# Kernel optimization log

Hardware: AMD Instinct MI355X
Metric: run time of the kernel (lower is better)

The kernel has to match this reference:

```python
import jax, jax.numpy as jnp
import numpy as np

IN_C, HID, OUT_C = 768, 568, 1024
EPS = 1e-5

def _ln(x, g, b):
    mu = jnp.mean(x, axis=-1, keepdims=True)
    var = jnp.var(x, axis=-1, keepdims=True)
    return (x - mu) / jnp.sqrt(var + EPS) * g + b

def setup_inputs() -> dict:
    key = jax.random.key(0)
    ks = jax.random.split(key, 20)
    def lin(k, fan_in, fan_out):
        bound = 1.0 / np.sqrt(fan_in)
        kw, kb = jax.random.split(k)
        w = jax.random.uniform(kw, (fan_in, fan_out), jnp.float32, -bound, bound)
        b = jax.random.uniform(kb, (fan_out,), jnp.float32, -bound, bound)
        return w, b
    x = jax.random.normal(ks[0], (4, 2048, IN_C), jnp.float32)
    w_mlp, b_mlp = lin(ks[1], IN_C, HID)
    wq, bq = lin(ks[2], HID, OUT_C)
    wk, bk = lin(ks[3], HID, OUT_C)
    wv, bv = lin(ks[4], HID, OUT_C)
    wm, bm = lin(ks[5], HID, OUT_C)
    wf1, bf1 = lin(ks[6], OUT_C, OUT_C)
    wf2, bf2 = lin(ks[7], OUT_C, OUT_C)
    g1 = jnp.ones((OUT_C,), jnp.float32); be1 = jnp.zeros((OUT_C,), jnp.float32)
    g2 = jnp.ones((OUT_C,), jnp.float32); be2 = jnp.zeros((OUT_C,), jnp.float32)
    return dict(x=x, w_mlp=w_mlp, b_mlp=b_mlp, wq=wq, bq=bq, wk=wk, bk=bk,
                wv=wv, bv=bv, wm=wm, bm=bm, g1=g1, be1=be1,
                wf1=wf1, bf1=bf1, wf2=wf2, bf2=bf2, g2=g2, be2=be2)

def reference(x, w_mlp, b_mlp, wq, bq, wk, bk, wv, bv, wm, bm,
              g1, be1, wf1, bf1, wf2, bf2, g2, be2):
    # Joint.mlp: Linear + ReLU  -> h: [B, S, HID]
    h = jax.nn.relu(jnp.einsum('bsi,ih->bsh', x, w_mlp) + b_mlp)
    # Block: single-head attention (dropout=eval -> identity)
    q = jnp.einsum('bsh,hd->bsd', h, wq) + bq
    k = jnp.einsum('bsh,hd->bsd', h, wk) + bk
    v = jnp.einsum('bsh,hd->bsd', h, wv) + bv
    scale = 1.0 / jnp.sqrt(jnp.float32(OUT_C))
    attn = jax.nn.softmax(jnp.einsum('bqd,bkd->bqk', q, k) * scale, axis=-1)
    attn_out = jnp.einsum('bqk,bkd->bqd', attn, v)
    x_mod = jnp.einsum('bsh,hd->bsd', h, wm) + bm
    x1 = _ln(x_mod + attn_out, g1, be1)
    ffn = jnp.einsum('bsd,de->bse', jax.nn.relu(jnp.einsum('bsd,de->bse', x1, wf1) + bf1), wf2) + bf2
    x2 = _ln(x1 + ffn, g2, be2)
    # trailing ReLU in Joint.attn Sequential
    return jax.nn.relu(x2)
```

## Files before the change

### kernel.cpp

```cpp
#include <hip/hip_runtime.h>

#define DI __device__ __forceinline__

typedef unsigned short u16;
typedef __attribute__((__ext_vector_type__(8))) __bf16 bf16x8;
typedef __attribute__((__ext_vector_type__(4))) float f32x4;
typedef __attribute__((__ext_vector_type__(4))) unsigned short u16x4;
typedef __attribute__((__ext_vector_type__(8))) unsigned short u16x8;

DI float bf2f(u16 u) { union { unsigned int i; float f; } x; x.i = ((unsigned int)u) << 16; return x.f; }
DI u16 f2bf(float f) {
  union { float f; unsigned int i; } x; x.f = f;
  unsigned int r = x.i + 0x7fffu + ((x.i >> 16) & 1u);
  return (u16)(r >> 16);
}

DI void gload_lds16(const void* g, void* lds) {
  __builtin_amdgcn_global_load_lds((const __attribute__((address_space(1))) unsigned int*)g,
                                   (__attribute__((address_space(3))) unsigned int*)lds, 16, 0, 0);
}

template<bool RELU, bool OUT_BF16, bool HAS_BIAS>
__global__ __launch_bounds__(512, 2)
void gemm256v2(const u16* __restrict__ A, long long sAb, int lda,
               const u16* __restrict__ Bt, long long sBb, int ldb,
               const float* __restrict__ bias,
               void* __restrict__ C, long long sCb, int ldc,
               int K, float scale)
{
  extern __shared__ __align__(16) u16 lds[];

  const int tid = threadIdx.x;
  const int w = tid >> 6, l = tid & 63;
  const int wm = w >> 2, wn = w & 3;

  const int gx = gridDim.x;
  const int nwg = gx * gridDim.y;
  const int f = blockIdx.x + gx * blockIdx.y;
  const int fs = (f & 7) * (nwg >> 3) + (f >> 3);
  const int bx = fs % gx, by = fs / gx;

  const long long bm = (long long)by * 256;
  const long long bn = (long long)bx * 256;
  const u16* Ab = A + (long long)blockIdx.z * sAb;
  const u16* Btb = Bt + (long long)blockIdx.z * sBb;

  const int trow = tid >> 3;
  const int tg = (tid & 7) ^ (trow & 7);
  const u16* sA = Ab + (bm + trow) * (long long)lda + tg * 8;
  const u16* sB = Btb + (bn + trow) * (long long)ldb + tg * 8;
  const long long la64 = (long long)64 * lda, lb64 = (long long)64 * ldb;

  const int swz0 = (((l >> 4) ^ (l & 7))) * 8;
  const int aB = (wm * 128 + (l & 15)) * 64;
  const int bB = 16384 + (wn * 64 + (l & 15)) * 64;

  f32x4 acc[8][4] = {};
  const int NKT = K >> 6;

  {
    u16* sp = lds;
    gload_lds16(sA, sp + w * 512);
    gload_lds16(sA + 2 * la64, sp + 8192 + w * 512);
    gload_lds16(sB, sp + 16384 + w * 512);
    gload_lds16(sB + lb64, sp + 20480 + w * 512);
    gload_lds16(sB + 2 * lb64, sp + 24576 + w * 512);
    gload_lds16(sB + 3 * lb64, sp + 28672 + w * 512);
    gload_lds16(sA + la64, sp + 4096 + w * 512);
    gload_lds16(sA + 3 * la64, sp + 12288 + w * 512);
  }

  for (int kt = 0; kt < NKT; ++kt) {
    const u16* bp = lds + (kt & 1) * 32768;
    u16* sp = lds + ((kt & 1) ^ 1) * 32768;
    const bool st = (kt + 1) < NKT;
    const long long ko = (long long)(kt + 1) * 64;

    asm volatile("s_waitcnt vmcnt(2)" ::: "memory");
    __builtin_amdgcn_s_barrier();

    if (st) {
      gload_lds16(sA + ko, sp + w * 512);
      gload_lds16(sA + 2 * la64 + ko, sp + 8192 + w * 512);
      gload_lds16(sB + ko, sp + 16384 + w * 512);
      gload_lds16(sB + lb64 + ko, sp + 20480 + w * 512);
      gload_lds16(sB + 2 * lb64 + ko, sp + 24576 + w * 512);
      gload_lds16(sB + 3 * lb64 + ko, sp + 28672 + w * 512);
    }

    bf16x8 bF[4][2], aF[4][2];
    #pragma unroll
    for (int nf = 0; nf < 4; ++nf) {
      bF[nf][0] = *(const bf16x8*)(bp + bB + nf * 1024 + swz0);
      bF[nf][1] = *(const bf16x8*)(bp + bB + nf * 1024 + (swz0 ^ 32));
    }
    #pragma unroll
    for (int mf = 0; mf < 4; ++mf) {
      aF[mf][0] = *(const bf16x8*)(bp + aB + mf * 1024 + swz0);
      aF[mf][1] = *(const bf16x8*)(bp + aB + mf * 1024 + (swz0 ^ 32));
    }
    if (st) {
      gload_lds16(sA + la64 + ko, sp + 4096 + w * 512);
      gload_lds16(sA + 3 * la64 + ko, sp + 12288 + w * 512);
    }
    __builtin_amdgcn_s_setprio(1);
    #pragma unroll
    for (int mf = 0; mf < 4; ++mf)
      #pragma unroll
      for (int nf = 0; nf < 4; ++nf) {
        acc[mf][nf] = __builtin_amdgcn_mfma_f32_16x16x32_bf16(aF[mf][0], bF[nf][0], acc[mf][nf], 0, 0, 0);
        acc[mf][nf] = __builtin_amdgcn_mfma_f32_16x16x32_bf16(aF[mf][1], bF[nf][1], acc[mf][nf], 0, 0, 0);
      }
    __builtin_amdgcn_s_setprio(0);

    if (st) asm volatile("s_waitcnt vmcnt(8)" ::: "memory");
    else    asm volatile("s_waitcnt vmcnt(0)" ::: "memory");
    __builtin_amdgcn_s_barrier();

    #pragma unroll
    for (int mf = 0; mf < 4; ++mf) {
      aF[mf][0] = *(const bf16x8*)(bp + aB + (mf + 4) * 1024 + swz0);
      aF[mf][1] = *(const bf16x8*)(bp + aB + (mf + 4) * 1024 + (swz0 ^ 32));
    }
    __builtin_amdgcn_s_setprio(1);
    #pragma unroll
    for (int mf = 0; mf < 4; ++mf)
      #pragma unroll
      for (int nf = 0; nf < 4; ++nf) {
        acc[mf + 4][nf] = __builtin_amdgcn_mfma_f32_16x16x32_bf16(aF[mf][0], bF[nf][0], acc[mf + 4][nf], 0, 0, 0);
        acc[mf + 4][nf] = __builtin_amdgcn_mfma_f32_16x16x32_bf16(aF[mf][1], bF[nf][1], acc[mf + 4][nf], 0, 0, 0);
      }
    __builtin_amdgcn_s_setprio(0);
  }

  __syncthreads();
  float bias4[4];
  if (HAS_BIAS) {
    #pragma unroll
    for (int nf = 0; nf < 4; ++nf) bias4[nf] = bias[bn + wn * 64 + (l & 15) + nf * 16];
  }
  float* fl = (float*)lds + w * 1024;
  const long long cbase = (long long)blockIdx.z * sCb;
  const int colq = (l & 15) * 4;
  #pragma unroll
  for (int mf = 0; mf < 8; ++mf) {
    #pragma unroll
    for (int nf = 0; nf < 4; ++nf) {
      #pragma unroll
      for (int r = 0; r < 4; ++r) {
        float v = acc[mf][nf][r] * scale;
        if (HAS_BIAS) v += bias4[nf];
        if (RELU) v = fmaxf(v, 0.f);
        fl[((l >> 4) * 4 + r) * 64 + (l & 15) + nf * 16] = v;
      }
    }
    asm volatile("s_waitcnt lgkmcnt(0)" ::: "memory");
    #pragma unroll
    for (int p = 0; p < 4; ++p) {
      f32x4 v = *(const f32x4*)(fl + p * 256 + l * 4);
      const long long row = bm + wm * 128 + mf * 16 + p * 4 + (l >> 4);
      const long long cidx = cbase + row * ldc + bn + wn * 64 + colq;
      if (OUT_BF16) {
        u16x4 o; o.x = f2bf(v.x); o.y = f2bf(v.y); o.z = f2bf(v.z); o.w = f2bf(v.w);
        *(u16x4*)((u16*)C + cidx) = o;
      } else {
        *(f32x4*)((float*)C + cidx) = v;
      }
    }
    asm volatile("s_waitcnt lgkmcnt(0)" ::: "memory");
  }
}

template<bool RELU, bool OUT_BF16, bool HAS_BIAS>
__global__ __launch_bounds__(512, 4)
void gemm128(const u16* __restrict__ A, long long sAb, int lda,
             const u16* __restrict__ Bt, long long sBb, int ldb,
             const float* __restrict__ bias,
             void* __restrict__ C, long long sCb, int ldc,
             int K, float scale)
{
  __shared__ __align__(16) u16 lds[24576];

  const int tid = threadIdx.x;
  const int w = tid >> 6, l = tid & 63;
  const int wm = w >> 2, wn = w & 3;

  const int gx = gridDim.x;
  const int nwg = gx * gridDim.y;
  const int f = blockIdx.x + gx * blockIdx.y;
  const int fs = (f & 7) * (nwg >> 3) + (f >> 3);
  const int bx = fs % gx, by = fs / gx;

  const long long bm = (long long)by * 128;
  const long long bn = (long long)bx * 256;
  const u16* Ab = A + (long long)blockIdx.z * sAb;
  const u16* Btb = Bt + (long long)blockIdx.z * sBb;

  const int ia = w * 64 + l;
  const int ra = ia >> 2;
  const int ga = (ia & 3) ^ ((ra >> 1) & 3);
  const u16* pA  = Ab  + (bm + ra) * (long long)lda + ga * 8;
  const u16* pB0 = Btb + (bn + ra) * (long long)ldb + ga * 8;
  const u16* pB1 = Btb + (bn + 128 + ra) * (long long)ldb + ga * 8;
  u16* dA  = lds + w * 512;
  u16* dB0 = lds + 4096 + w * 512;
  u16* dB1 = lds + 8192 + w * 512;

  const int swz = ((l >> 4) ^ (((l & 15) >> 1) & 3)) << 3;
  const int aOff = (wm * 64 + (l & 15)) * 32 + swz;
  const int bOff = 4096 + (wn * 64 + (l & 15)) * 32 + swz;

  f32x4 acc[4][4] = {};
  const int NKT = K >> 5;

  gload_lds16(pA, dA);        gload_lds16(pB0, dB0);        gload_lds16(pB1, dB1);
  gload_lds16(pA + 32, dA + 12288); gload_lds16(pB0 + 32, dB0 + 12288); gload_lds16(pB1 + 32, dB1 + 12288);

  for (int kt = 0; kt < NKT; ++kt) {
    if (kt + 1 < NKT) asm volatile("s_waitcnt vmcnt(3)" ::: "memory");
    else              asm volatile("s_waitcnt vmcnt(0)" ::: "memory");
    __builtin_amdgcn_s_barrier();
    __builtin_amdgcn_sched_barrier(0);

    const u16* bufc = lds + (kt & 1) * 12288;
    bf16x8 aF[4], bF[4];
    #pragma unroll
    for (int mf = 0; mf < 4; ++mf) aF[mf] = *(const bf16x8*)(bufc + aOff + mf * 512);
    #pragma unroll
    for (int nf = 0; nf < 4; ++nf) bF[nf] = *(const bf16x8*)(bufc + bOff + nf * 512);
    asm volatile("s_waitcnt lgkmcnt(0)" ::: "memory");
    __builtin_amdgcn_s_barrier();
    __builtin_amdgcn_sched_barrier(0);

    if (kt + 2 < NKT) {
      u16* d = lds + (kt & 1) * 12288 + w * 512;
      const long long ko = (long long)(kt + 2) * 32;
      gload_lds16(pA + ko, d);
      gload_lds16(pB0 + ko, d + 4096);
      gload_lds16(pB1 + ko, d + 8192);
    }
    __builtin_amdgcn_s_setprio(1);
    #pragma unroll
    for (int mf = 0; mf < 4; ++mf)
      #pragma unroll
      for (int nf = 0; nf < 4; ++nf)
        acc[mf][nf] = __builtin_amdgcn_mfma_f32_16x16x32_bf16(aF[mf], bF[nf], acc[mf][nf], 0, 0, 0);
    __builtin_amdgcn_s_setprio(0);
  }

  float bias4[4];
  if (HAS_BIAS) {
    #pragma unroll
    for (int nf = 0; nf < 4; ++nf) bias4[nf] = bias[bn + wn * 64 + (l & 15) + nf * 16];
  }
  float* fl = (float*)lds + w * 1024;
  const long long cbase = (long long)blockIdx.z * sCb;
  const int colq = (l & 15) * 4;
  #pragma unroll
  for (int mf = 0; mf < 4; ++mf) {
    #pragma unroll
    for (int nf = 0; nf < 4; ++nf) {
      #pragma unroll
      for (int r = 0; r < 4; ++r) {
        float v = acc[mf][nf][r] * scale;
        if (HAS_BIAS) v += bias4[nf];
        if (RELU) v = fmaxf(v, 0.f);
        fl[((l >> 4) * 4 + r) * 64 + (l & 15) + nf * 16] = v;
      }
    }
    asm volatile("s_waitcnt lgkmcnt(0)" ::: "memory");
    #pragma unroll
    for (int p = 0; p < 4; ++p) {
      f32x4 v = *(const f32x4*)(fl + p * 256 + l * 4);
      const long long row = bm + wm * 64 + mf * 16 + p * 4 + (l >> 4);
      const long long cidx = cbase + row * ldc + bn + wn * 64 + colq;
      if (OUT_BF16) {
        u16x4 o; o.x = f2bf(v.x); o.y = f2bf(v.y); o.z = f2bf(v.z); o.w = f2bf(v.w);
        *(u16x4*)((u16*)C + cidx) = o;
      } else {
        *(f32x4*)((float*)C + cidx) = v;
      }
    }
    asm volatile("s_waitcnt lgkmcnt(0)" ::: "memory");
  }
}

__global__ void transpose_cast_pad(const float* __restrict__ in, int inR, int inC,
                                   u16* __restrict__ out, int outR, int outC)
{
  __shared__ float tile[32][33];
  const int c0 = blockIdx.x * 32;
  const int r0 = blockIdx.y * 32;
  const int tx = threadIdx.x, ty = threadIdx.y;
  for (int i = ty; i < 32; i += 8) {
    int r = r0 + i, c = c0 + tx;
    tile[i][tx] = (r < inR && c < inC) ? in[(long long)r * inC + c] : 0.f;
  }
  __syncthreads();
  for (int i = ty; i < 32; i += 8) {
    int orow = c0 + i, ocol = r0 + tx;
    if (orow < outR && ocol < outC)
      out[(long long)orow * outC + ocol] = f2bf(tile[tx][i]);
  }
}

__global__ void transpose_bf16_k(const u16* __restrict__ in, long long sIb, int ldi,
                                 u16* __restrict__ out, long long sOb, int ldo)
{
  __shared__ u16 tile[32][33];
  const u16* inp = in + (long long)blockIdx.z * sIb;
  u16* outp = out + (long long)blockIdx.z * sOb;
  const int r0 = blockIdx.y * 32, c0 = blockIdx.x * 32;
  const int tx = threadIdx.x, ty = threadIdx.y;
  for (int i = ty; i < 32; i += 8)
    tile[i][tx] = inp[(long long)(r0 + i) * ldi + c0 + tx];
  __syncthreads();
  for (int i = ty; i < 32; i += 8)
    outp[(long long)(c0 + i) * ldo + r0 + tx] = tile[tx][i];
}

__global__ void cast_f32_bf16_k(const float* __restrict__ in, u16* __restrict__ out, int n4)
{
  int i = blockIdx.x * blockDim.x + threadIdx.x;
  if (i >= n4) return;
  float4 v = ((const float4*)in)[i];
  u16x4 o; o.x = f2bf(v.x); o.y = f2bf(v.y); o.z = f2bf(v.z); o.w = f2bf(v.w);
  ((u16x4*)out)[i] = o;
}

__global__ void prep_bias_k(const float* __restrict__ bmlp, const float* __restrict__ bq,
                            const float* __restrict__ bk, const float* __restrict__ bv,
                            const float* __restrict__ bm,
                            float* __restrict__ outMlp, float* __restrict__ outQkvm)
{
  int i = blockIdx.x * 256 + threadIdx.x;
  if (i < 768) outMlp[i] = (i < 568) ? bmlp[i] : 0.f;
  if (i < 4096) {
    const float* s = (i < 1024) ? bq : (i < 2048) ? bk : (i < 3072) ? bv : bm;
    outQkvm[i] = s[i & 1023];
  }
}

__global__ __launch_bounds__(256)
void softmax_rows_k(u16* __restrict__ sc)
{
  __shared__ float red[8];
  const long long base = (long long)blockIdx.x * 2048;
  const int t = threadIdx.x, wave = t >> 6, lane = t & 63;
  u16x8 v8 = *((const u16x8*)(sc + base + t * 8));
  float v[8];
  #pragma unroll
  for (int j = 0; j < 8; ++j) v[j] = bf2f(v8[j]);
  float m = v[0];
  #pragma unroll
  for (int j = 1; j < 8; ++j) m = fmaxf(m, v[j]);
  #pragma unroll
  for (int off = 32; off > 0; off >>= 1) m = fmaxf(m, __shfl_xor(m, off, 64));
  if (lane == 0) red[wave] = m;
  __syncthreads();
  m = fmaxf(fmaxf(red[0], red[1]), fmaxf(red[2], red[3]));
  float s = 0.f;
  #pragma unroll
  for (int j = 0; j < 8; ++j) { v[j] = __expf(v[j] - m); s += v[j]; }
  #pragma unroll
  for (int off = 32; off > 0; off >>= 1) s += __shfl_xor(s, off, 64);
  if (lane == 0) red[4 + wave] = s;
  __syncthreads();
  s = red[4] + red[5] + red[6] + red[7];
  float inv = 1.f / s;
  u16x8 o;
  #pragma unroll
  for (int j = 0; j < 8; ++j) o[j] = f2bf(v[j] * inv);
  *((u16x8*)(sc + base + t * 8)) = o;
}

__global__ __launch_bounds__(256)
void add_ln_k(const u16* __restrict__ a, int lda, const float* __restrict__ b,
              const float* __restrict__ gamma, const float* __restrict__ beta,
              u16* __restrict__ out)
{
  __shared__ float red[8];
  const long long row = blockIdx.x;
  const int t = threadIdx.x, wave = t >> 6, lane = t & 63;
  u16x4 av = *((const u16x4*)(a + row * lda + t * 4));
  float4 bv = ((const float4*)(b + row * 1024))[t];
  float z[4] = { bf2f(av.x) + bv.x, bf2f(av.y) + bv.y, bf2f(av.z) + bv.z, bf2f(av.w) + bv.w };
  float s = z[0] + z[1] + z[2] + z[3];
  float ss = z[0]*z[0] + z[1]*z[1] + z[2]*z[2] + z[3]*z[3];
  #pragma unroll
  for (int off = 32; off > 0; off >>= 1) { s += __shfl_xor(s, off, 64); ss += __shfl_xor(ss, off, 64); }
  if (lane == 0) { red[wave] = s; red[4 + wave] = ss; }
  __syncthreads();
  s = red[0] + red[1] + red[2] + red[3];
  ss = red[4] + red[5] + red[6] + red[7];
  float mu = s * (1.f / 1024.f);
  float var = ss * (1.f / 1024.f) - mu * mu;
  float rstd = rsqrtf(var + 1e-5f);
  float4 g = ((const float4*)gamma)[t];
  float4 be = ((const float4*)beta)[t];
  u16x4 o;
  o.x = f2bf((z[0] - mu) * rstd * g.x + be.x);
  o.y = f2bf((z[1] - mu) * rstd * g.y + be.y);
  o.z = f2bf((z[2] - mu) * rstd * g.z + be.z);
  o.w = f2bf((z[3] - mu) * rstd * g.w + be.w);
  *((u16x4*)(out + row * 1024 + t * 4)) = o;
}

__global__ __launch_bounds__(256)
void add_ln_relu_k(const u16* __restrict__ a, const float* __restrict__ b,
                   const float* __restrict__ gamma, const float* __restrict__ beta,
                   float* __restrict__ out)
{
  __shared__ float red[8];
  const long long row = blockIdx.x;
  const int t = threadIdx.x, wave = t >> 6, lane = t & 63;
  u16x4 av = *((const u16x4*)(a + row * 1024 + t * 4));
  float4 bv = ((const float4*)(b + row * 1024))[t];
  float z[4] = { bf2f(av.x) + bv.x, bf2f(av.y) + bv.y, bf2f(av.z) + bv.z, bf2f(av.w) + bv.w };
  float s = z[0] + z[1] + z[2] + z[3];
  float ss = z[0]*z[0] + z[1]*z[1] + z[2]*z[2] + z[3]*z[3];
  #pragma unroll
  for (int off = 32; off > 0; off >>= 1) { s += __shfl_xor(s, off, 64); ss += __shfl_xor(ss, off, 64); }
  if (lane == 0) { red[wave] = s; red[4 + wave] = ss; }
  __syncthreads();
  s = red[0] + red[1] + red[2] + red[3];
  ss = red[4] + red[5] + red[6] + red[7];
  float mu = s * (1.f / 1024.f);
  float var = ss * (1.f / 1024.f) - mu * mu;
  float rstd = rsqrtf(var + 1e-5f);
  float4 g = ((const float4*)gamma)[t];
  float4 be = ((const float4*)beta)[t];
  float4 o;
  o.x = fmaxf((z[0] - mu) * rstd * g.x + be.x, 0.f);
  o.y = fmaxf((z[1] - mu) * rstd * g.y + be.y, 0.f);
  o.z = fmaxf((z[2] - mu) * rstd * g.z + be.z, 0.f);
  o.w = fmaxf((z[3] - mu) * rstd * g.w + be.w, 0.f);
  ((float4*)(out + row * 1024))[t] = o;
}

extern "C" void kernel_launch(void* const* d_in, const int* in_sizes, int n_in,
                              void* d_out, int out_size, void* d_ws, size_t ws_size,
                              hipStream_t stream)
{
  const float* x    = (const float*)d_in[0];
  const float* wmlp = (const float*)d_in[1];
  const float* bmlp = (const float*)d_in[2];
  const float* wq   = (const float*)d_in[3];  const float* bq  = (const float*)d_in[4];
  const float* wk   = (const float*)d_in[5];  const float* bk  = (const float*)d_in[6];
  const float* wv   = (const float*)d_in[7];  const float* bv  = (const float*)d_in[8];
  const float* wm   = (const float*)d_in[9];  const float* bm  = (const float*)d_in[10];
  const float* g1   = (const float*)d_in[11]; const float* be1 = (const float*)d_in[12];
  const float* wf1  = (const float*)d_in[13]; const float* bf1 = (const float*)d_in[14];
  const float* wf2  = (const float*)d_in[15]; const float* bf2 = (const float*)d_in[16];
  const float* g2   = (const float*)d_in[17]; const float* be2 = (const float*)d_in[18];

  char* ws = (char*)d_ws;
  size_t off = 0;
  auto alloc = [&](size_t bytes) { char* p = ws + off; off += (bytes + 255) & ~(size_t)255; return p; };
  u16*  W_MLP_T  = (u16*)alloc((size_t)768 * 768 * 2);
  u16*  W_QKVM_T = (u16*)alloc((size_t)4096 * 640 * 2);
  u16*  W_F1_T   = (u16*)alloc((size_t)1024 * 1024 * 2);
  u16*  W_F2_T   = (u16*)alloc((size_t)1024 * 1024 * 2);
  float* B_MLP   = (float*)alloc(768 * 4);
  float* B_QKVM  = (float*)alloc(4096 * 4);
  u16*  XBF      = (u16*)alloc((size_t)8192 * 768 * 2);
  u16*  H        = (u16*)alloc((size_t)8192 * 768 * 2);
  u16*  QKVM     = (u16*)alloc((size_t)8192 * 4096 * 2);
  u16*  VT       = (u16*)alloc((size_t)4 * 1024 * 2048 * 2);
  u16*  SC       = (u16*)alloc((size_t)4 * 2048 * 2048 * 2);
  float* AO      = (float*)alloc((size_t)8192 * 1024 * 4);
  u16*  X1       = (u16*)alloc((size_t)8192 * 1024 * 2);
  u16*  T  = QKVM;
  float* F = (float*)((char*)QKVM + (size_t)8192 * 2048 * 2);

  hipFuncSetAttribute((const void*)gemm256v2<false, true, true >, hipFuncAttributeMaxDynamicSharedMemorySize, 131072);
  hipFuncSetAttribute((const void*)gemm256v2<false, true, false>, hipFuncAttributeMaxDynamicSharedMemorySize, 131072);

  dim3 tb(32, 8);

  cast_f32_bf16_k<<<(8192 * 768 / 4 + 255) / 256, 256, 0, stream>>>(x, XBF, 8192 * 768 / 4);
  transpose_cast_pad<<<dim3(24, 24), tb, 0, stream>>>(wmlp, 768, 568, W_MLP_T, 768, 768);
  transpose_cast_pad<<<dim3(32, 20), tb, 0, stream>>>(wq, 568, 1024, W_QKVM_T + (size_t)0 * 1024 * 640, 1024, 640);
  transpose_cast_pad<<<dim3(32, 20), tb, 0, stream>>>(wk, 568, 1024, W_QKVM_T + (size_t)1 * 1024 * 640, 1024, 640);
  transpose_cast_pad<<<dim3(32, 20), tb, 0, stream>>>(wv, 568, 1024, W_QKVM_T + (size_t)2 * 1024 * 640, 1024, 640);
  transpose_cast_pad<<<dim3(32, 20), tb, 0, stream>>>(wm, 568, 1024, W_QKVM_T + (size_t)3 * 1024 * 640, 1024, 640);
  transpose_cast_pad<<<dim3(32, 32), tb, 0, stream>>>(wf1, 1024, 1024, W_F1_T, 1024, 1024);
  transpose_cast_pad<<<dim3(32, 32), tb, 0, stream>>>(wf2, 1024, 1024, W_F2_T, 1024, 1024);
  prep_bias_k<<<16, 256, 0, stream>>>(bmlp, bq, bk, bv, bm, B_MLP, B_QKVM);

  gemm128<true, true, true><<<dim3(3, 64, 1), 512, 0, stream>>>(
      XBF, 0, 768, W_MLP_T, 0, 768, B_MLP, H, 0, 768, 768, 1.0f);
  gemm256v2<false, true, true><<<dim3(16, 32, 1), 512, 131072, stream>>>(
      H, 0, 768, W_QKVM_T, 0, 640, B_QKVM, QKVM, 0, 4096, 640, 1.0f);
  transpose_bf16_k<<<dim3(32, 64, 4), tb, 0, stream>>>(
      QKVM + 2048, (long long)2048 * 4096, 4096, VT, (long long)1024 * 2048, 2048);
  gemm256v2<false, true, false><<<dim3(8, 8, 4), 512, 131072, stream>>>(
      QKVM, (long long)2048 * 4096, 4096, QKVM + 1024, (long long)2048 * 4096, 4096,
      nullptr, SC, (long long)2048 * 2048, 2048, 1024, 0.03125f);
  softmax_rows_k<<<8192, 256, 0, stream>>>(SC);
  gemm128<false, false, false><<<dim3(4, 16, 4), 512, 0, stream>>>(
      SC, (long long)2048 * 2048, 2048, VT, (long long)1024 * 2048, 2048,
      nullptr, AO, (long long)2048 * 1024, 1024, 2048, 1.0f);
  add_ln_k<<<8192, 256, 0, stream>>>(QKVM + 3072, 4096, AO, g1, be1, X1);
  gemm128<true, true, true><<<dim3(4, 64, 1), 512, 0, stream>>>(
      X1, 0, 1024, W_F1_T, 0, 1024, bf1, T, 0, 1024, 1024, 1.0f);
  gemm128<false, false, true><<<dim3(4, 64, 1), 512, 0, stream>>>(
      T, 0, 1024, W_F2_T, 0, 1024, bf2, F, 0, 1024, 1024, 1.0f);
  add_ln_relu_k<<<8192, 256, 0, stream>>>(X1, F, g2, be2, (float*)d_out);
}
```

Measured before the change: 281.2 us.

## Restructure 256-tile GEMM into 8-phase pipeline, swizzle epilogue LDS, store bf16 intermediates

The 256x256 GEMM main loop is split into four sub-phases per K tile, each loading two A fragments and issuing staggered global-to-LDS prefetches, with B prefetched two tiles ahead. The goal is to interleave memory traffic with MFMA work more finely. Both GEMM epilogues now XOR-swizzle the LDS staging buffer to avoid bank conflicts. The attention output and FFN2 output are written as bf16 instead of fp32, halving their traffic into the layernorm kernels at the cost of some precision.

```diff
diff --git a/kernel.cpp b/kernel.cpp
--- a/kernel.cpp
+++ b/kernel.cpp
@@ -20,13 +20,15 @@
                                    (__attribute__((address_space(3))) unsigned int*)lds, 16, 0, 0);
 }
 
+#define MFMA16(a, b, c) __builtin_amdgcn_mfma_f32_16x16x32_bf16((a), (b), (c), 0, 0, 0)
+
 template<bool RELU, bool OUT_BF16, bool HAS_BIAS>
 __global__ __launch_bounds__(512, 2)
-void gemm256v2(const u16* __restrict__ A, long long sAb, int lda,
-               const u16* __restrict__ Bt, long long sBb, int ldb,
-               const float* __restrict__ bias,
-               void* __restrict__ C, long long sCb, int ldc,
-               int K, float scale)
+void gemm8p(const u16* __restrict__ A, long long sAb, int lda,
+            const u16* __restrict__ Bt, long long sBb, int ldb,
+            const float* __restrict__ bias,
+            void* __restrict__ C, long long sCb, int ldc,
+            int K, float scale)
 {
   extern __shared__ __align__(16) u16 lds[];
 
@@ -47,93 +49,132 @@
 
   const int trow = tid >> 3;
   const int tg = (tid & 7) ^ (trow & 7);
-  const u16* sA = Ab + (bm + trow) * (long long)lda + tg * 8;
-  const u16* sB = Btb + (bn + trow) * (long long)ldb + tg * 8;
-  const long long la64 = (long long)64 * lda, lb64 = (long long)64 * ldb;
-
-  const int swz0 = (((l >> 4) ^ (l & 7))) * 8;
-  const int aB = (wm * 128 + (l & 15)) * 64;
-  const int bB = 16384 + (wn * 64 + (l & 15)) * 64;
+  const u16* gA = Ab + (bm + trow) * (long long)lda + tg * 8;
+  const u16* gB = Btb + (bn + trow) * (long long)ldb + tg * 8;
+  const long long a64 = (long long)64 * lda, b64 = (long long)64 * ldb;
+  const int wlds = w * 512;
+
+  const int slot0 = ((l >> 4) ^ (l & 7)) * 8;
+  const int aRow = (wm * 128 + (l & 15)) * 64;
+  const int bRow = 16384 + (wn * 64 + (l & 15)) * 64;
 
   f32x4 acc[8][4] = {};
   const int NKT = K >> 6;
 
-  {
-    u16* sp = lds;
-    gload_lds16(sA, sp + w * 512);
-    gload_lds16(sA + 2 * la64, sp + 8192 + w * 512);
-    gload_lds16(sB, sp + 16384 + w * 512);
-    gload_lds16(sB + lb64, sp + 20480 + w * 512);
-    gload_lds16(sB + 2 * lb64, sp + 24576 + w * 512);
-    gload_lds16(sB + 3 * lb64, sp + 28672 + w * 512);
-    gload_lds16(sA + la64, sp + 4096 + w * 512);
-    gload_lds16(sA + 3 * la64, sp + 12288 + w * 512);
-  }
-
-  for (int kt = 0; kt < NKT; ++kt) {
-    const u16* bp = lds + (kt & 1) * 32768;
-    u16* sp = lds + ((kt & 1) ^ 1) * 32768;
-    const bool st = (kt + 1) < NKT;
-    const long long ko = (long long)(kt + 1) * 64;
-
-    asm volatile("s_waitcnt vmcnt(2)" ::: "memory");
-    __builtin_amdgcn_s_barrier();
-
-    if (st) {
-      gload_lds16(sA + ko, sp + w * 512);
-      gload_lds16(sA + 2 * la64 + ko, sp + 8192 + w * 512);
-      gload_lds16(sB + ko, sp + 16384 + w * 512);
-      gload_lds16(sB + lb64 + ko, sp + 20480 + w * 512);
-      gload_lds16(sB + 2 * lb64 + ko, sp + 24576 + w * 512);
-      gload_lds16(sB + 3 * lb64 + ko, sp + 28672 + w * 512);
+  gload_lds16(gB,             lds + 16384 + wlds);
+  gload_lds16(gB + b64,       lds + 16384 + 4096 + wlds);
+  gload_lds16(gB + 2 * b64,   lds + 16384 + 8192 + wlds);
+  gload_lds16(gB + 3 * b64,   lds + 16384 + 12288 + wlds);
+  gload_lds16(gA,             lds + wlds);
+  gload_lds16(gA + a64,       lds + 4096 + wlds);
+  gload_lds16(gA + 2 * a64,   lds + 8192 + wlds);
+  gload_lds16(gA + 3 * a64,   lds + 12288 + wlds);
+  if (NKT > 1) {
+    gload_lds16(gB + 64,           lds + 32768 + 16384 + wlds);
+    gload_lds16(gB + b64 + 64,     lds + 32768 + 16384 + 4096 + wlds);
+    gload_lds16(gB + 2 * b64 + 64, lds + 32768 + 16384 + 8192 + wlds);
+    gload_lds16(gB + 3 * b64 + 64, lds + 32768 + 16384 + 12288 + wlds);
+    asm volatile("s_waitcnt vmcnt(4)" ::: "memory");
+  } else {
+    asm volatile("s_waitcnt vmcnt(0)" ::: "memory");
+  }
+  __builtin_amdgcn_s_barrier();
+
+  for (int t = 0; t < NKT; ++t) {
+    const u16* bp = lds + (t & 1) * 32768;
+    u16* cur = lds + (t & 1) * 32768;
+    u16* oth = lds + ((t + 1) & 1) * 32768;
+    const long long koA = (long long)(t + 1) * 64;
+    const long long koB = (long long)(t + 2) * 64;
+    const bool stA = (t + 1) < NKT;
+    const bool stB = (t + 2) < NKT;
+
+    bf16x8 bF[4][2], aF[2][2];
+
+    #pragma unroll
+    for (int nf = 0; nf < 4; ++nf) {
+      bF[nf][0] = *(const bf16x8*)(bp + bRow + nf * 1024 + slot0);
+      bF[nf][1] = *(const bf16x8*)(bp + bRow + nf * 1024 + (slot0 ^ 32));
     }
-
-    bf16x8 bF[4][2], aF[4][2];
-    #pragma unroll
-    for (int nf = 0; nf < 4; ++nf) {
-      bF[nf][0] = *(const bf16x8*)(bp + bB + nf * 1024 + swz0);
-      bF[nf][1] = *(const bf16x8*)(bp + bB + nf * 1024 + (swz0 ^ 32));
-    }
-    #pragma unroll
-    for (int mf = 0; mf < 4; ++mf) {
-      aF[mf][0] = *(const bf16x8*)(bp + aB + mf * 1024 + swz0);
-      aF[mf][1] = *(const bf16x8*)(bp + aB + mf * 1024 + (swz0 ^ 32));
-    }
-    if (st) {
-      gload_lds16(sA + la64 + ko, sp + 4096 + w * 512);
-      gload_lds16(sA + 3 * la64 + ko, sp + 12288 + w * 512);
-    }
+    aF[0][0] = *(const bf16x8*)(bp + aRow + slot0);
+    aF[0][1] = *(const bf16x8*)(bp + aRow + (slot0 ^ 32));
+    aF[1][0] = *(const bf16x8*)(bp + aRow + 1024 + slot0);
+    aF[1][1] = *(const bf16x8*)(bp + aRow + 1024 + (slot0 ^ 32));
+    if (stA) { gload_lds16(gA + koA, oth + wlds); gload_lds16(gA + a64 + koA, oth + 4096 + wlds); }
+    __builtin_amdgcn_s_barrier();
+    asm volatile("s_waitcnt lgkmcnt(0)" ::: "memory");
+    __builtin_amdgcn_sched_barrier(0);
     __builtin_amdgcn_s_setprio(1);
     #pragma unroll
-    for (int mf = 0; mf < 4; ++mf)
+    for (int mf = 0; mf < 2; ++mf)
       #pragma unroll
       for (int nf = 0; nf < 4; ++nf) {
-        acc[mf][nf] = __builtin_amdgcn_mfma_f32_16x16x32_bf16(aF[mf][0], bF[nf][0], acc[mf][nf], 0, 0, 0);
-        acc[mf][nf] = __builtin_amdgcn_mfma_f32_16x16x32_bf16(aF[mf][1], bF[nf][1], acc[mf][nf], 0, 0, 0);
+        acc[mf][nf] = MFMA16(aF[mf][0], bF[nf][0], acc[mf][nf]);
+        acc[mf][nf] = MFMA16(aF[mf][1], bF[nf][1], acc[mf][nf]);
       }
     __builtin_amdgcn_s_setprio(0);
-
-    if (st) asm volatile("s_waitcnt vmcnt(8)" ::: "memory");
-    else    asm volatile("s_waitcnt vmcnt(0)" ::: "memory");
-    __builtin_amdgcn_s_barrier();
-
-    #pragma unroll
-    for (int mf = 0; mf < 4; ++mf) {
-      aF[mf][0] = *(const bf16x8*)(bp + aB + (mf + 4) * 1024 + swz0);
-      aF[mf][1] = *(const bf16x8*)(bp + aB + (mf + 4) * 1024 + (swz0 ^ 32));
-    }
+    __builtin_amdgcn_s_barrier();
+
+    aF[0][0] = *(const bf16x8*)(bp + aRow + 2048 + slot0);
+    aF[0][1] = *(const bf16x8*)(bp + aRow + 2048 + (slot0 ^ 32));
+    aF[1][0] = *(const bf16x8*)(bp + aRow + 3072 + slot0);
+    aF[1][1] = *(const bf16x8*)(bp + aRow + 3072 + (slot0 ^ 32));
+    if (stA) { gload_lds16(gA + 2 * a64 + koA, oth + 8192 + wlds); gload_lds16(gA + 3 * a64 + koA, oth + 12288 + wlds); }
+    __builtin_amdgcn_s_barrier();
+    asm volatile("s_waitcnt lgkmcnt(0)" ::: "memory");
+    __builtin_amdgcn_sched_barrier(0);
     __builtin_amdgcn_s_setprio(1);
     #pragma unroll
-    for (int mf = 0; mf < 4; ++mf)
+    for (int mf = 0; mf < 2; ++mf)
       #pragma unroll
       for (int nf = 0; nf < 4; ++nf) {
-        acc[mf + 4][nf] = __builtin_amdgcn_mfma_f32_16x16x32_bf16(aF[mf][0], bF[nf][0], acc[mf + 4][nf], 0, 0, 0);
-        acc[mf + 4][nf] = __builtin_amdgcn_mfma_f32_16x16x32_bf16(aF[mf][1], bF[nf][1], acc[mf + 4][nf], 0, 0, 0);
+        acc[mf + 2][nf] = MFMA16(aF[mf][0], bF[nf][0], acc[mf + 2][nf]);
+        acc[mf + 2][nf] = MFMA16(aF[mf][1], bF[nf][1], acc[mf + 2][nf]);
       }
     __builtin_amdgcn_s_setprio(0);
-  }
-
-  __syncthreads();
+    __builtin_amdgcn_s_barrier();
+
+    aF[0][0] = *(const bf16x8*)(bp + aRow + 4096 + slot0);
+    aF[0][1] = *(const bf16x8*)(bp + aRow + 4096 + (slot0 ^ 32));
+    aF[1][0] = *(const bf16x8*)(bp + aRow + 5120 + slot0);
+    aF[1][1] = *(const bf16x8*)(bp + aRow + 5120 + (slot0 ^ 32));
+    if (stB) { gload_lds16(gB + koB, cur + 16384 + wlds); gload_lds16(gB + b64 + koB, cur + 16384 + 4096 + wlds); }
+    __builtin_amdgcn_s_barrier();
+    asm volatile("s_waitcnt lgkmcnt(0)" ::: "memory");
+    __builtin_amdgcn_sched_barrier(0);
+    __builtin_amdgcn_s_setprio(1);
+    #pragma unroll
+    for (int mf = 0; mf < 2; ++mf)
+      #pragma unroll
+      for (int nf = 0; nf < 4; ++nf) {
+        acc[mf + 4][nf] = MFMA16(aF[mf][0], bF[nf][0], acc[mf + 4][nf]);
+        acc[mf + 4][nf] = MFMA16(aF[mf][1], bF[nf][1], acc[mf + 4][nf]);
+      }
+    __builtin_amdgcn_s_setprio(0);
+    __builtin_amdgcn_s_barrier();
+
+    aF[0][0] = *(const bf16x8*)(bp + aRow + 6144 + slot0);
+    aF[0][1] = *(const bf16x8*)(bp + aRow + 6144 + (slot0 ^ 32));
+    aF[1][0] = *(const bf16x8*)(bp + aRow + 7168 + slot0);
+    aF[1][1] = *(const bf16x8*)(bp + aRow + 7168 + (slot0 ^ 32));
+    if (stB) { gload_lds16(gB + 2 * b64 + koB, cur + 16384 + 8192 + wlds); gload_lds16(gB + 3 * b64 + koB, cur + 16384 + 12288 + wlds); }
+    __builtin_amdgcn_s_barrier();
+    asm volatile("s_waitcnt lgkmcnt(0)" ::: "memory");
+    __builtin_amdgcn_sched_barrier(0);
+    __builtin_amdgcn_s_setprio(1);
+    #pragma unroll
+    for (int mf = 0; mf < 2; ++mf)
+      #pragma unroll
+      for (int nf = 0; nf < 4; ++nf) {
+        acc[mf + 6][nf] = MFMA16(aF[mf][0], bF[nf][0], acc[mf + 6][nf]);
+        acc[mf + 6][nf] = MFMA16(aF[mf][1], bF[nf][1], acc[mf + 6][nf]);
+      }
+    __builtin_amdgcn_s_setprio(0);
+    if (stB)      asm volatile("s_waitcnt vmcnt(4)" ::: "memory");
+    else if (stA) asm volatile("s_waitcnt vmcnt(0)" ::: "memory");
+    __builtin_amdgcn_s_barrier();
+  }
+
   float bias4[4];
   if (HAS_BIAS) {
     #pragma unroll
@@ -141,7 +182,7 @@
   }
   float* fl = (float*)lds + w * 1024;
   const long long cbase = (long long)blockIdx.z * sCb;
-  const int colq = (l & 15) * 4;
+  const int q = l >> 4;
   #pragma unroll
   for (int mf = 0; mf < 8; ++mf) {
     #pragma unroll
@@ -151,15 +192,15 @@
         float v = acc[mf][nf][r] * scale;
         if (HAS_BIAS) v += bias4[nf];
         if (RELU) v = fmaxf(v, 0.f);
-        fl[((l >> 4) * 4 + r) * 64 + (l & 15) + nf * 16] = v;
+        fl[(q * 4 + r) * 64 + ((((l & 15) + nf * 16)) ^ (q << 4))] = v;
       }
     }
     asm volatile("s_waitcnt lgkmcnt(0)" ::: "memory");
     #pragma unroll
     for (int p = 0; p < 4; ++p) {
-      f32x4 v = *(const f32x4*)(fl + p * 256 + l * 4);
-      const long long row = bm + wm * 128 + mf * 16 + p * 4 + (l >> 4);
-      const long long cidx = cbase + row * ldc + bn + wn * 64 + colq;
+      f32x4 v = *(const f32x4*)(fl + (p * 4 + q) * 64 + (((l & 15) * 4) ^ (p << 4)));
+      const long long row = bm + wm * 128 + mf * 16 + p * 4 + q;
+      const long long cidx = cbase + row * ldc + bn + wn * 64 + (l & 15) * 4;
       if (OUT_BF16) {
         u16x4 o; o.x = f2bf(v.x); o.y = f2bf(v.y); o.z = f2bf(v.z); o.w = f2bf(v.w);
         *(u16x4*)((u16*)C + cidx) = o;
@@ -244,7 +285,7 @@
     for (int mf = 0; mf < 4; ++mf)
       #pragma unroll
       for (int nf = 0; nf < 4; ++nf)
-        acc[mf][nf] = __builtin_amdgcn_mfma_f32_16x16x32_bf16(aF[mf], bF[nf], acc[mf][nf], 0, 0, 0);
+        acc[mf][nf] = MFMA16(aF[mf], bF[nf], acc[mf][nf]);
     __builtin_amdgcn_s_setprio(0);
   }
 
@@ -255,7 +296,7 @@
   }
   float* fl = (float*)lds + w * 1024;
   const long long cbase = (long long)blockIdx.z * sCb;
-  const int colq = (l & 15) * 4;
+  const int q = l >> 4;
   #pragma unroll
   for (int mf = 0; mf < 4; ++mf) {
     #pragma unroll
@@ -265,15 +306,15 @@
         float v = acc[mf][nf][r] * scale;
         if (HAS_BIAS) v += bias4[nf];
         if (RELU) v = fmaxf(v, 0.f);
-        fl[((l >> 4) * 4 + r) * 64 + (l & 15) + nf * 16] = v;
+        fl[(q * 4 + r) * 64 + ((((l & 15) + nf * 16)) ^ (q << 4))] = v;
       }
     }
     asm volatile("s_waitcnt lgkmcnt(0)" ::: "memory");
     #pragma unroll
     for (int p = 0; p < 4; ++p) {
-      f32x4 v = *(const f32x4*)(fl + p * 256 + l * 4);
-      const long long row = bm + wm * 64 + mf * 16 + p * 4 + (l >> 4);
-      const long long cidx = cbase + row * ldc + bn + wn * 64 + colq;
+      f32x4 v = *(const f32x4*)(fl + (p * 4 + q) * 64 + (((l & 15) * 4) ^ (p << 4)));
+      const long long row = bm + wm * 64 + mf * 16 + p * 4 + q;
+      const long long cidx = cbase + row * ldc + bn + wn * 64 + (l & 15) * 4;
       if (OUT_BF16) {
         u16x4 o; o.x = f2bf(v.x); o.y = f2bf(v.y); o.z = f2bf(v.z); o.w = f2bf(v.w);
         *(u16x4*)((u16*)C + cidx) = o;
@@ -375,7 +416,7 @@
 }
 
 __global__ __launch_bounds__(256)
-void add_ln_k(const u16* __restrict__ a, int lda, const float* __restrict__ b,
+void add_ln_k(const u16* __restrict__ a, int lda, const u16* __restrict__ b,
               const float* __restrict__ gamma, const float* __restrict__ beta,
               u16* __restrict__ out)
 {
@@ -383,8 +424,9 @@
   const long long row = blockIdx.x;
   const int t = threadIdx.x, wave = t >> 6, lane = t & 63;
   u16x4 av = *((const u16x4*)(a + row * lda + t * 4));
-  float4 bv = ((const float4*)(b + row * 1024))[t];
-  float z[4] = { bf2f(av.x) + bv.x, bf2f(av.y) + bv.y, bf2f(av.z) + bv.z, bf2f(av.w) + bv.w };
+  u16x4 bv = *((const u16x4*)(b + row * 1024 + t * 4));
+  float z[4] = { bf2f(av.x) + bf2f(bv.x), bf2f(av.y) + bf2f(bv.y),
+                 bf2f(av.z) + bf2f(bv.z), bf2f(av.w) + bf2f(bv.w) };
   float s = z[0] + z[1] + z[2] + z[3];
   float ss = z[0]*z[0] + z[1]*z[1] + z[2]*z[2] + z[3]*z[3];
   #pragma unroll
@@ -407,7 +449,7 @@
 }
 
 __global__ __launch_bounds__(256)
-void add_ln_relu_k(const u16* __restrict__ a, const float* __restrict__ b,
+void add_ln_relu_k(const u16* __restrict__ a, const u16* __restrict__ b,
                    const float* __restrict__ gamma, const float* __restrict__ beta,
                    float* __restrict__ out)
 {
@@ -415,8 +457,9 @@
   const long long row = blockIdx.x;
   const int t = threadIdx.x, wave = t >> 6, lane = t & 63;
   u16x4 av = *((const u16x4*)(a + row * 1024 + t * 4));
-  float4 bv = ((const float4*)(b + row * 1024))[t];
-  float z[4] = { bf2f(av.x) + bv.x, bf2f(av.y) + bv.y, bf2f(av.z) + bv.z, bf2f(av.w) + bv.w };
+  u16x4 bv = *((const u16x4*)(b + row * 1024 + t * 4));
+  float z[4] = { bf2f(av.x) + bf2f(bv.x), bf2f(av.y) + bf2f(bv.y),
+                 bf2f(av.z) + bf2f(bv.z), bf2f(av.w) + bf2f(bv.w) };
   float s = z[0] + z[1] + z[2] + z[3];
   float ss = z[0]*z[0] + z[1]*z[1] + z[2]*z[2] + z[3]*z[3];
   #pragma unroll
@@ -468,13 +511,13 @@
   u16*  QKVM     = (u16*)alloc((size_t)8192 * 4096 * 2);
   u16*  VT       = (u16*)alloc((size_t)4 * 1024 * 2048 * 2);
   u16*  SC       = (u16*)alloc((size_t)4 * 2048 * 2048 * 2);
-  float* AO      = (float*)alloc((size_t)8192 * 1024 * 4);
+  u16*  AO       = (u16*)alloc((size_t)8192 * 1024 * 2);
   u16*  X1       = (u16*)alloc((size_t)8192 * 1024 * 2);
   u16*  T  = QKVM;
-  float* F = (float*)((char*)QKVM + (size_t)8192 * 2048 * 2);
-
-  hipFuncSetAttribute((const void*)gemm256v2<false, true, true >, hipFuncAttributeMaxDynamicSharedMemorySize, 131072);
-  hipFuncSetAttribute((const void*)gemm256v2<false, true, false>, hipFuncAttributeMaxDynamicSharedMemorySize, 131072);
+  u16*  F  = QKVM + (size_t)8192 * 1024;
+
+  hipFuncSetAttribute((const void*)gemm8p<false, true, true >, hipFuncAttributeMaxDynamicSharedMemorySize, 131072);
+  hipFuncSetAttribute((const void*)gemm8p<false, true, false>, hipFuncAttributeMaxDynamicSharedMemorySize, 131072);
 
   dim3 tb(32, 8);
 
@@ -490,21 +533,21 @@
 
   gemm128<true, true, true><<<dim3(3, 64, 1), 512, 0, stream>>>(
       XBF, 0, 768, W_MLP_T, 0, 768, B_MLP, H, 0, 768, 768, 1.0f);
-  gemm256v2<false, true, true><<<dim3(16, 32, 1), 512, 131072, stream>>>(
+  gemm8p<false, true, true><<<dim3(16, 32, 1), 512, 131072, stream>>>(
       H, 0, 768, W_QKVM_T, 0, 640, B_QKVM, QKVM, 0, 4096, 640, 1.0f);
   transpose_bf16_k<<<dim3(32, 64, 4), tb, 0, stream>>>(
       QKVM + 2048, (long long)2048 * 4096, 4096, VT, (long long)1024 * 2048, 2048);
-  gemm256v2<false, true, false><<<dim3(8, 8, 4), 512, 131072, stream>>>(
+  gemm8p<false, true, false><<<dim3(8, 8, 4), 512, 131072, stream>>>(
       QKVM, (long long)2048 * 4096, 4096, QKVM + 1024, (long long)2048 * 4096, 4096,
       nullptr, SC, (long long)2048 * 2048, 2048, 1024, 0.03125f);
   softmax_rows_k<<<8192, 256, 0, stream>>>(SC);
-  gemm128<false, false, false><<<dim3(4, 16, 4), 512, 0, stream>>>(
+  gemm128<false, true, false><<<dim3(4, 16, 4), 512, 0, stream>>>(
       SC, (long long)2048 * 2048, 2048, VT, (long long)1024 * 2048, 2048,
       nullptr, AO, (long long)2048 * 1024, 1024, 2048, 1.0f);
   add_ln_k<<<8192, 256, 0, stream>>>(QKVM + 3072, 4096, AO, g1, be1, X1);
   gemm128<true, true, true><<<dim3(4, 64, 1), 512, 0, stream>>>(
       X1, 0, 1024, W_F1_T, 0, 1024, bf1, T, 0, 1024, 1024, 1.0f);
-  gemm128<false, false, true><<<dim3(4, 64, 1), 512, 0, stream>>>(
+  gemm128<false, true, true><<<dim3(4, 64, 1), 512, 0, stream>>>(
       T, 0, 1024, W_F2_T, 0, 1024, bf2, F, 0, 1024, 1024, 1.0f);
   add_ln_relu_k<<<8192, 256, 0, stream>>>(X1, F, g2, be2, (float*)d_out);
 }
```

After: 276.4 us. Within noise of the previous version (-1.7%).

## Store AO and FFN outputs as bf16, swizzle epilogue LDS, raise gemm128 occupancy

Applied to the files above, without the earlier changes.

The attention-output and FFN2 GEMMs now write bf16 instead of fp32, and the following add+LayerNorm kernels read bf16. This halves the intermediate write and read traffic. The per-wave epilogue LDS staging uses an XOR swizzle to cut bank conflicts, and gemm128's launch bounds rise from 4 to 6 waves/SIMD hint, which may force register spills. The bf16 intermediates also lose precision before LayerNorm.

```diff
diff --git a/kernel.cpp b/kernel.cpp
--- a/kernel.cpp
+++ b/kernel.cpp
@@ -19,6 +19,8 @@
   __builtin_amdgcn_global_load_lds((const __attribute__((address_space(1))) unsigned int*)g,
                                    (__attribute__((address_space(3))) unsigned int*)lds, 16, 0, 0);
 }
+
+#define MFMA16(a, b, c) __builtin_amdgcn_mfma_f32_16x16x32_bf16((a), (b), (c), 0, 0, 0)
 
 template<bool RELU, bool OUT_BF16, bool HAS_BIAS>
 __global__ __launch_bounds__(512, 2)
@@ -108,8 +110,8 @@
     for (int mf = 0; mf < 4; ++mf)
       #pragma unroll
       for (int nf = 0; nf < 4; ++nf) {
-        acc[mf][nf] = __builtin_amdgcn_mfma_f32_16x16x32_bf16(aF[mf][0], bF[nf][0], acc[mf][nf], 0, 0, 0);
-        acc[mf][nf] = __builtin_amdgcn_mfma_f32_16x16x32_bf16(aF[mf][1], bF[nf][1], acc[mf][nf], 0, 0, 0);
+        acc[mf][nf] = MFMA16(aF[mf][0], bF[nf][0], acc[mf][nf]);
+        acc[mf][nf] = MFMA16(aF[mf][1], bF[nf][1], acc[mf][nf]);
       }
     __builtin_amdgcn_s_setprio(0);
 
@@ -127,8 +129,8 @@
     for (int mf = 0; mf < 4; ++mf)
       #pragma unroll
       for (int nf = 0; nf < 4; ++nf) {
-        acc[mf + 4][nf] = __builtin_amdgcn_mfma_f32_16x16x32_bf16(aF[mf][0], bF[nf][0], acc[mf + 4][nf], 0, 0, 0);
-        acc[mf + 4][nf] = __builtin_amdgcn_mfma_f32_16x16x32_bf16(aF[mf][1], bF[nf][1], acc[mf + 4][nf], 0, 0, 0);
+        acc[mf + 4][nf] = MFMA16(aF[mf][0], bF[nf][0], acc[mf + 4][nf]);
+        acc[mf + 4][nf] = MFMA16(aF[mf][1], bF[nf][1], acc[mf + 4][nf]);
       }
     __builtin_amdgcn_s_setprio(0);
   }
@@ -141,7 +143,7 @@
   }
   float* fl = (float*)lds + w * 1024;
   const long long cbase = (long long)blockIdx.z * sCb;
-  const int colq = (l & 15) * 4;
+  const int q = l >> 4;
   #pragma unroll
   for (int mf = 0; mf < 8; ++mf) {
     #pragma unroll
@@ -151,15 +153,15 @@
         float v = acc[mf][nf][r] * scale;
         if (HAS_BIAS) v += bias4[nf];
         if (RELU) v = fmaxf(v, 0.f);
-        fl[((l >> 4) * 4 + r) * 64 + (l & 15) + nf * 16] = v;
+        fl[(q * 4 + r) * 64 + ((((l & 15) + nf * 16)) ^ (q << 4))] = v;
       }
     }
     asm volatile("s_waitcnt lgkmcnt(0)" ::: "memory");
     #pragma unroll
     for (int p = 0; p < 4; ++p) {
-      f32x4 v = *(const f32x4*)(fl + p * 256 + l * 4);
-      const long long row = bm + wm * 128 + mf * 16 + p * 4 + (l >> 4);
-      const long long cidx = cbase + row * ldc + bn + wn * 64 + colq;
+      f32x4 v = *(const f32x4*)(fl + (p * 4 + q) * 64 + (((l & 15) * 4) ^ (p << 4)));
+      const long long row = bm + wm * 128 + mf * 16 + p * 4 + q;
+      const long long cidx = cbase + row * ldc + bn + wn * 64 + (l & 15) * 4;
       if (OUT_BF16) {
         u16x4 o; o.x = f2bf(v.x); o.y = f2bf(v.y); o.z = f2bf(v.z); o.w = f2bf(v.w);
         *(u16x4*)((u16*)C + cidx) = o;
@@ -172,7 +174,7 @@
 }
 
 template<bool RELU, bool OUT_BF16, bool HAS_BIAS>
-__global__ __launch_bounds__(512, 4)
+__global__ __launch_bounds__(512, 6)
 void gemm128(const u16* __restrict__ A, long long sAb, int lda,
              const u16* __restrict__ Bt, long long sBb, int ldb,
              const float* __restrict__ bias,
@@ -244,7 +246,7 @@
     for (int mf = 0; mf < 4; ++mf)
       #pragma unroll
       for (int nf = 0; nf < 4; ++nf)
-        acc[mf][nf] = __builtin_amdgcn_mfma_f32_16x16x32_bf16(aF[mf], bF[nf], acc[mf][nf], 0, 0, 0);
+        acc[mf][nf] = MFMA16(aF[mf], bF[nf], acc[mf][nf]);
     __builtin_amdgcn_s_setprio(0);
   }
 
@@ -255,7 +257,7 @@
   }
   float* fl = (float*)lds + w * 1024;
   const long long cbase = (long long)blockIdx.z * sCb;
-  const int colq = (l & 15) * 4;
+  const int q = l >> 4;
   #pragma unroll
   for (int mf = 0; mf < 4; ++mf) {
     #pragma unroll
@@ -265,15 +267,15 @@
         float v = acc[mf][nf][r] * scale;
         if (HAS_BIAS) v += bias4[nf];
         if (RELU) v = fmaxf(v, 0.f);
-        fl[((l >> 4) * 4 + r) * 64 + (l & 15) + nf * 16] = v;
+        fl[(q * 4 + r) * 64 + ((((l & 15) + nf * 16)) ^ (q << 4))] = v;
       }
     }
     asm volatile("s_waitcnt lgkmcnt(0)" ::: "memory");
     #pragma unroll
     for (int p = 0; p < 4; ++p) {
-      f32x4 v = *(const f32x4*)(fl + p * 256 + l * 4);
-      const long long row = bm + wm * 64 + mf * 16 + p * 4 + (l >> 4);
-      const long long cidx = cbase + row * ldc + bn + wn * 64 + colq;
+      f32x4 v = *(const f32x4*)(fl + (p * 4 + q) * 64 + (((l & 15) * 4) ^ (p << 4)));
+      const long long row = bm + wm * 64 + mf * 16 + p * 4 + q;
+      const long long cidx = cbase + row * ldc + bn + wn * 64 + (l & 15) * 4;
       if (OUT_BF16) {
         u16x4 o; o.x = f2bf(v.x); o.y = f2bf(v.y); o.z = f2bf(v.z); o.w = f2bf(v.w);
         *(u16x4*)((u16*)C + cidx) = o;
@@ -375,7 +377,7 @@
 }
 
 __global__ __launch_bounds__(256)
-void add_ln_k(const u16* __restrict__ a, int lda, const float* __restrict__ b,
+void add_ln_k(const u16* __restrict__ a, int lda, const u16* __restrict__ b,
               const float* __restrict__ gamma, const float* __restrict__ beta,
               u16* __restrict__ out)
 {
@@ -383,8 +385,9 @@
   const long long row = blockIdx.x;
   const int t = threadIdx.x, wave = t >> 6, lane = t & 63;
   u16x4 av = *((const u16x4*)(a + row * lda + t * 4));
-  float4 bv = ((const float4*)(b + row * 1024))[t];
-  float z[4] = { bf2f(av.x) + bv.x, bf2f(av.y) + bv.y, bf2f(av.z) + bv.z, bf2f(av.w) + bv.w };
+  u16x4 bv = *((const u16x4*)(b + row * 1024 + t * 4));
+  float z[4] = { bf2f(av.x) + bf2f(bv.x), bf2f(av.y) + bf2f(bv.y),
+                 bf2f(av.z) + bf2f(bv.z), bf2f(av.w) + bf2f(bv.w) };
   float s = z[0] + z[1] + z[2] + z[3];
   float ss = z[0]*z[0] + z[1]*z[1] + z[2]*z[2] + z[3]*z[3];
   #pragma unroll
@@ -407,7 +410,7 @@
 }
 
 __global__ __launch_bounds__(256)
-void add_ln_relu_k(const u16* __restrict__ a, const float* __restrict__ b,
+void add_ln_relu_k(const u16* __restrict__ a, const u16* __restrict__ b,
                    const float* __restrict__ gamma, const float* __restrict__ beta,
                    float* __restrict__ out)
 {
@@ -415,8 +418,9 @@
   const long long row = blockIdx.x;
   const int t = threadIdx.x, wave = t >> 6, lane = t & 63;
   u16x4 av = *((const u16x4*)(a + row * 1024 + t * 4));
-  float4 bv = ((const float4*)(b + row * 1024))[t];
-  float z[4] = { bf2f(av.x) + bv.x, bf2f(av.y) + bv.y, bf2f(av.z) + bv.z, bf2f(av.w) + bv.w };
+  u16x4 bv = *((const u16x4*)(b + row * 1024 + t * 4));
+  float z[4] = { bf2f(av.x) + bf2f(bv.x), bf2f(av.y) + bf2f(bv.y),
+                 bf2f(av.z) + bf2f(bv.z), bf2f(av.w) + bf2f(bv.w) };
   float s = z[0] + z[1] + z[2] + z[3];
   float ss = z[0]*z[0] + z[1]*z[1] + z[2]*z[2] + z[3]*z[3];
   #pragma unroll
@@ -468,10 +472,10 @@
   u16*  QKVM     = (u16*)alloc((size_t)8192 * 4096 * 2);
   u16*  VT       = (u16*)alloc((size_t)4 * 1024 * 2048 * 2);
   u16*  SC       = (u16*)alloc((size_t)4 * 2048 * 2048 * 2);
-  float* AO      = (float*)alloc((size_t)8192 * 1024 * 4);
+  u16*  AO       = (u16*)alloc((size_t)8192 * 1024 * 2);
   u16*  X1       = (u16*)alloc((size_t)8192 * 1024 * 2);
   u16*  T  = QKVM;
-  float* F = (float*)((char*)QKVM + (size_t)8192 * 2048 * 2);
+  u16*  F  = QKVM + (size_t)8192 * 1024;
 
   hipFuncSetAttribute((const void*)gemm256v2<false, true, true >, hipFuncAttributeMaxDynamicSharedMemorySize, 131072);
   hipFuncSetAttribute((const void*)gemm256v2<false, true, false>, hipFuncAttributeMaxDynamicSharedMemorySize, 131072);
@@ -498,13 +502,13 @@
       QKVM, (long long)2048 * 4096, 4096, QKVM + 1024, (long long)2048 * 4096, 4096,
       nullptr, SC, (long long)2048 * 2048, 2048, 1024, 0.03125f);
   softmax_rows_k<<<8192, 256, 0, stream>>>(SC);
-  gemm128<false, false, false><<<dim3(4, 16, 4), 512, 0, stream>>>(
+  gemm128<false, true, false><<<dim3(4, 16, 4), 512, 0, stream>>>(
       SC, (long long)2048 * 2048, 2048, VT, (long long)1024 * 2048, 2048,
       nullptr, AO, (long long)2048 * 1024, 1024, 2048, 1.0f);
   add_ln_k<<<8192, 256, 0, stream>>>(QKVM + 3072, 4096, AO, g1, be1, X1);
   gemm128<true, true, true><<<dim3(4, 64, 1), 512, 0, stream>>>(
       X1, 0, 1024, W_F1_T, 0, 1024, bf1, T, 0, 1024, 1024, 1.0f);
-  gemm128<false, false, true><<<dim3(4, 64, 1), 512, 0, stream>>>(
+  gemm128<false, true, true><<<dim3(4, 64, 1), 512, 0, stream>>>(
       T, 0, 1024, W_F2_T, 0, 1024, bf2, F, 0, 1024, 1024, 1.0f);
   add_ln_relu_k<<<8192, 256, 0, stream>>>(X1, F, g2, be2, (float*)d_out);
 }
```

New measurement: 880.4 us. +213.1%, slower.
